# Performance work log

Measured on AMD Instinct MI355X. Metric: run time of the kernel, lower is better.

Reference implementation:

```python
import jax, jax.numpy as jnp
import numpy as np
import math

HEADS = 16
MAX_LEN = 512  # tokens; seq must equal this for the relative bias to be valid
D_HEAD = 64
BH = 256  # batch*heads


def setup_inputs() -> dict:
    key = jax.random.key(0)
    k1, k2, k3, k4 = jax.random.split(key, 4)
    S, B, D = MAX_LEN, BH, D_HEAD
    return {
        "query": jax.random.normal(k1, (S, B, D), dtype=jnp.float32),
        "key": jax.random.normal(k2, (S, B, D), dtype=jnp.float32),
        "value": jax.random.normal(k3, (S, B, D), dtype=jnp.float32),
        # per-head relative position embedding table [heads, 2*tokens-1, d_head]
        "k_rpos_emb": jax.random.normal(k4, (HEADS, 2 * MAX_LEN - 1, D), dtype=jnp.float32),
    }


def reference(query, key, value, k_rpos_emb):
    # 'seq b f -> b seq f'
    q = jnp.transpose(query, (1, 0, 2))   # [bh, s, d]
    k = jnp.transpose(key, (1, 0, 2))
    v = jnp.transpose(value, (1, 0, 2))
    bh, s, d = q.shape
    b = bh // HEADS

    # relative position bias from keys: split heads, contract with per-head table
    kh = k.reshape(b, HEADS, s, d)                                   # [b,h,s,d]
    rel_logits = jnp.einsum('bhid,hrd->bhir', kh, k_rpos_emb)        # [b,h,s,2L-1]
    rel_idx = (jnp.arange(s)[None, :] - jnp.arange(s)[:, None]
               + MAX_LEN - 1).astype(jnp.int32)                      # [s,s] in [0,2L-2]
    rel_bias = jnp.take_along_axis(
        rel_logits, rel_idx[None, None, :, :], axis=-1)              # [b,h,s,s]
    rel_bias = rel_bias.reshape(bh, s, s)

    scale = 1.0 / math.sqrt(d)
    scores = (jnp.einsum('bid,bjd->bij', q, k) + rel_bias) * scale   # [bh,s,s]
    attn = jax.nn.softmax(scores, axis=-1)
    out = jnp.einsum('bij,bjd->bid', attn, v)                        # [bh,s,d]
    return jnp.transpose(out, (1, 0, 2))                             # [s,bh,d]
```

## Files before the change

### kernel.cpp

```cpp
#include <hip/hip_runtime.h>
#include <hip/hip_bf16.h>

#define S_LEN  512
#define D_DIM  64
#define NH     16
#define R_LEN  1023
#define BHD    16384
#define PPITCH 68
#define SCL2   0.1803368801111204f
#define DTHR   8.0f

typedef __attribute__((ext_vector_type(8))) short   short8_t;
typedef __attribute__((ext_vector_type(8))) __bf16  bf16x8;
typedef __attribute__((ext_vector_type(4))) float   floatx4;

__device__ __forceinline__ unsigned short f2bf(float f) {
  union { float f; unsigned u; } v; v.f = f;
  return (unsigned short)((v.u + 0x7fffu + ((v.u >> 16) & 1u)) >> 16);
}
__device__ __forceinline__ ushort2 c2(float x, float y) {
  __hip_bfloat162 h = __float22bfloat162_rn(float2{x, y});
  union { __hip_bfloat162 h; ushort2 u; } v; v.h = h; return v.u;
}
__device__ __forceinline__ unsigned c2u(float x, float y) {
  ushort2 u = c2(x, y);
  union { ushort2 u; unsigned w; } v; v.u = u; return v.w;
}
__device__ __forceinline__ short8_t pack8s(float4 a, float4 b) {
  union { ushort2 u2[4]; short8_t s8; } u;
  u.u2[0] = c2(a.x, a.y); u.u2[1] = c2(a.z, a.w);
  u.u2[2] = c2(b.x, b.y); u.u2[3] = c2(b.z, b.w);
  return u.s8;
}
__device__ __forceinline__ bf16x8 pack8(float4 a, float4 b) {
  short8_t s = pack8s(a, b);
  return __builtin_bit_cast(bf16x8, s);
}
__device__ __forceinline__ bf16x8 pack8scaled(float4 a, float4 b, float s) {
  a.x *= s; a.y *= s; a.z *= s; a.w *= s;
  b.x *= s; b.y *= s; b.z *= s; b.w *= s;
  return pack8(a, b);
}
__device__ __forceinline__ bf16x8 ldfrag(const unsigned short* p) {
  short8_t s = *(const short8_t*)p;
  return __builtin_bit_cast(bf16x8, s);
}
__device__ __forceinline__ bf16x8 ldfrag8(const unsigned short* p) {
  union { ushort4 u4[2]; short8_t s8; } u;
  u.u4[0] = *(const ushort4*)p;
  u.u4[1] = *(const ushort4*)(p + 4);
  return __builtin_bit_cast(bf16x8, u.s8);
}
__device__ __forceinline__ bf16x8 ldseg(const unsigned short* buf, int r, int seg) {
  return ldfrag(buf + r * 64 + ((seg ^ (r & 7)) << 3));
}
__device__ __forceinline__ void async16(const void* g, void* l) {
  __builtin_amdgcn_global_load_lds(
      (const __attribute__((address_space(1))) unsigned int*)(unsigned long long)(uintptr_t)g,
      (__attribute__((address_space(3))) unsigned int*)(unsigned int)(uintptr_t)l,
      16, 0, 0);
}
__device__ __forceinline__ void stage16(const unsigned short* gb, size_t rstride,
                                        unsigned short* lb, int lane) {
  int srow = lane >> 3;
  int sseg = (lane & 7) ^ srow;
  async16(gb + (size_t)srow * rstride + sseg * 8, lb);
  async16(gb + (size_t)(srow + 8) * rstride + sseg * 8, lb + 512);
}
__device__ __forceinline__ void stageE(const unsigned short* gb, int sigma,
                                       unsigned short* slot, int lane, int wv) {
  int srow = lane >> 3;
  int sseg = (lane & 7) ^ srow;
  int r0 = sigma * 64 + wv * 16 + srow;
  unsigned short* lb = slot + (wv * 16) * 64;
  async16(gb + (size_t)min(r0, R_LEN - 1) * D_DIM + sseg * 8, lb);
  async16(gb + (size_t)min(r0 + 8, R_LEN - 1) * D_DIM + sseg * 8, lb + 512);
}
template<int N>
__device__ __forceinline__ float dpp_ror(float x) {
  int i = __builtin_bit_cast(int, x);
  int r = __builtin_amdgcn_update_dpp(i, i, 0x120 + N, 0xF, 0xF, false);
  return __builtin_bit_cast(float, r);
}
__device__ __forceinline__ float rmax16(float x) {
  x = fmaxf(x, dpp_ror<8>(x)); x = fmaxf(x, dpp_ror<4>(x));
  x = fmaxf(x, dpp_ror<2>(x)); x = fmaxf(x, dpp_ror<1>(x));
  return x;
}
__device__ __forceinline__ float rsum16(float x) {
  x += dpp_ror<8>(x); x += dpp_ror<4>(x);
  x += dpp_ror<2>(x); x += dpp_ror<1>(x);
  return x;
}
__device__ __forceinline__ float fexp2(float x) {
#if __has_builtin(__builtin_amdgcn_exp2f)
  return __builtin_amdgcn_exp2f(x);
#else
  return exp2f(x);
#endif
}

extern "C" __global__ void prepass(const float* __restrict__ k, const float* __restrict__ v,
                                   const float* __restrict__ emb,
                                   unsigned short* __restrict__ kb,
                                   unsigned short* __restrict__ vtb,
                                   unsigned short* __restrict__ eb) {
  __shared__ unsigned tw[64 * 36];
  const int bid = blockIdx.x;
  const int tid = threadIdx.x;
  if (bid < 4096) {
    size_t i = (size_t)bid * 256 + tid;
    const float* s = k + i * 8;
    float4 a = *(const float4*)s, b = *(const float4*)(s + 4);
    *(short8_t*)(kb + i * 8) = pack8s(a, b);
  } else if (bid < 4608) {
    size_t i = (size_t)(bid - 4096) * 256 + tid;
    if (i < 130944) {
      const float* s = emb + i * 8;
      float4 a = *(const float4*)s, b = *(const float4*)(s + 4);
      bf16x8 r = pack8scaled(a, b, SCL2);
      *(short8_t*)(eb + i * 8) = __builtin_bit_cast(short8_t, r);
    }
  } else {
    const int b2 = bid - 4608;
    const int bh = b2 >> 3;
    const int j0 = (b2 & 7) << 6;
    for (int item = tid; item < 512; item += 256) {
      const int dg = item & 15;
      const int jp = item >> 4;
      const float* s0 = v + (size_t)(j0 + 2 * jp) * BHD + bh * D_DIM + dg * 4;
      float4 a = *(const float4*)s0;
      float4 b = *(const float4*)(s0 + BHD);
      const unsigned key = (unsigned)(dg & 7);
      const unsigned col = (unsigned)(jp & 3) | ((((unsigned)jp >> 2) ^ key) << 2);
      tw[(dg * 4 + 0) * 36 + col] = c2u(a.x, b.x);
      tw[(dg * 4 + 1) * 36 + col] = c2u(a.y, b.y);
      tw[(dg * 4 + 2) * 36 + col] = c2u(a.z, b.z);
      tw[(dg * 4 + 3) * 36 + col] = c2u(a.w, b.w);
    }
    __syncthreads();
    for (int item = tid; item < 512; item += 256) {
      const int d = item >> 3, jseg = item & 7;
      const unsigned key = ((unsigned)d >> 2) & 7;
      const unsigned* p = tw + d * 36 + (((unsigned)jseg ^ key) << 2);
      uint4 w = *(const uint4*)p;
      *(uint4*)(vtb + ((size_t)bh * D_DIM + d) * S_LEN + j0 + jseg * 8) = w;
    }
  }
}

extern "C" __global__ __launch_bounds__(256, 2)
void attn_relbias(const float* __restrict__ q, const unsigned short* __restrict__ kb,
                  const unsigned short* __restrict__ vtb,
                  const unsigned short* __restrict__ eb,
                  float* __restrict__ out)
{
  __shared__ unsigned short kbuf[2][4096];
  __shared__ unsigned short vbuf[2][4096];
  __shared__ unsigned short ebuf[4][4096];
  __shared__ unsigned short ps[4][16 * PPITCH];

  const int tid  = threadIdx.x;
  const int bh   = blockIdx.x & 255;
  const int i0   = (blockIdx.x >> 8) << 7;
  const int h    = bh & (NH - 1);
  const int wv   = tid >> 6;
  const int lane = tid & 63;
  const int l15  = lane & 15;
  const int quad = lane >> 4;
  const int iloc0 = wv * 16 + quad * 4;
  const int elo   = 3 - wv;
  const int arow  = wv * 16 + l15;
  const int acol  = quad * 8;
  const int it0   = 7 - (i0 >> 6);

  const unsigned short* kgb  = kb  + (size_t)bh * D_DIM;
  const unsigned short* vgb  = vtb + (size_t)bh * (D_DIM * S_LEN);
  const unsigned short* egb  = eb  + (size_t)h * (R_LEN * D_DIM);

  stage16(kgb + (size_t)(wv * 16) * BHD, BHD, &kbuf[0][(wv * 16) * 64], lane);
  stage16(vgb + (size_t)(wv * 16) * S_LEN, S_LEN, &vbuf[0][(wv * 16) * 64], lane);
  stageE(egb, it0 - 1, ebuf[(it0 - 1) & 3], lane, wv);
  stageE(egb, it0,     ebuf[it0 & 3],       lane, wv);
  stageE(egb, it0 + 1, ebuf[(it0 + 1) & 3], lane, wv);

  bf16x8 qa0[2], qa1[2], ia0[2], ia1[2];
  #pragma unroll
  for (int st = 0; st < 2; ++st) {
    const int row = i0 + st * 64 + arow;
    const float* gq = q + (size_t)row * BHD + bh * D_DIM + acol;
    qa0[st] = pack8scaled(*(const float4*)gq,        *(const float4*)(gq + 4), SCL2);
    qa1[st] = pack8scaled(*(const float4*)(gq + 32), *(const float4*)(gq + 36), SCL2);
    const unsigned short* gi = kb + (size_t)row * BHD + bh * D_DIM + acol;
    ia0[st] = ldfrag(gi);
    ia1[st] = ldfrag(gi + 32);
  }

  floatx4 oacc[2][4];
  float m_i[2][4], l_i[2][4];
  #pragma unroll
  for (int st = 0; st < 2; ++st) {
    #pragma unroll
    for (int r = 0; r < 4; ++r) {
      oacc[st][r] = (floatx4){0.f, 0.f, 0.f, 0.f};
      m_i[st][r] = -1e30f; l_i[st][r] = 0.f;
    }
  }

  __syncthreads();

  #pragma unroll 2
  for (int t = 0; t < 8; ++t) {
    if (t < 7) {
      const int j1 = t * 64 + 64;
      stage16(kgb + (size_t)(j1 + wv * 16) * BHD, BHD, &kbuf[(t + 1) & 1][(wv * 16) * 64], lane);
      stage16(vgb + (size_t)(wv * 16) * S_LEN + j1, S_LEN, &vbuf[(t + 1) & 1][(wv * 16) * 64], lane);
      stageE(egb, it0 + t + 2, ebuf[(it0 + t + 2) & 3], lane, wv);
    }
    const unsigned short* kc = kbuf[t & 1];
    const unsigned short* vc = vbuf[t & 1];

    floatx4 bacc[2][5];
    floatx4 qk[2][4];
    __builtin_amdgcn_s_setprio(1);
    #pragma unroll
    for (int st = 0; st < 2; ++st) {
      const int sbase = it0 - st + t;
      #pragma unroll
      for (int ei = 0; ei < 5; ++ei) {
        const int eblk = elo + ei;
        const unsigned short* es = ebuf[(sbase + (eblk >> 2)) & 3];
        const int lr = (eblk * 16 + l15) & 63;
        floatx4 bz = (floatx4){0.f, 0.f, 0.f, 0.f};
        bz = __builtin_amdgcn_mfma_f32_16x16x32_bf16(ia0[st], ldseg(es, lr, quad),     bz, 0, 0, 0);
        bz = __builtin_amdgcn_mfma_f32_16x16x32_bf16(ia1[st], ldseg(es, lr, quad + 4), bz, 0, 0, 0);
        bacc[st][ei] = bz;
      }
    }
    #pragma unroll
    for (int c = 0; c < 4; ++c) {
      bf16x8 k0 = ldseg(kc, c * 16 + l15, quad);
      bf16x8 k1 = ldseg(kc, c * 16 + l15, quad + 4);
      #pragma unroll
      for (int st = 0; st < 2; ++st) {
        floatx4 acc = (floatx4){0.f, 0.f, 0.f, 0.f};
        acc = __builtin_amdgcn_mfma_f32_16x16x32_bf16(qa0[st], k0, acc, 0, 0, 0);
        acc = __builtin_amdgcn_mfma_f32_16x16x32_bf16(qa1[st], k1, acc, 0, 0, 0);
        qk[st][c] = acc;
      }
    }
    __builtin_amdgcn_s_setprio(0);

    unsigned short* psw = ps[wv];
    bf16x8 vb0[4], vb1[4];
    #pragma unroll
    for (int st = 0; st < 2; ++st) {
      float sc[4][4];
      #pragma unroll
      for (int r = 0; r < 4; ++r) {
        const int o  = 15 - 4 * quad - r;
        const int ls = (lane & 48) + ((l15 + o) & 15);
        const bool hi = (l15 + o) >= 16;
        #pragma unroll
        for (int c = 0; c < 4; ++c) {
          float blo = __shfl(bacc[st][c][r],     ls);
          float bhi = __shfl(bacc[st][c + 1][r], ls);
          sc[c][r] = qk[st][c][r] + (hi ? bhi : blo);
        }
      }
      float mx4[4];
      #pragma unroll
      for (int r = 0; r < 4; ++r) {
        float mx = fmaxf(fmaxf(sc[0][r], sc[1][r]), fmaxf(sc[2][r], sc[3][r]));
        mx4[r] = rmax16(mx);
      }
      float dm = fmaxf(fmaxf(mx4[0] - m_i[st][0], mx4[1] - m_i[st][1]),
                       fmaxf(mx4[2] - m_i[st][2], mx4[3] - m_i[st][3]));
      float p[4][4];
      if (__all(dm <= DTHR)) {
        #pragma unroll
        for (int r = 0; r < 4; ++r) {
          float rs = 0.f;
          #pragma unroll
          for (int c = 0; c < 4; ++c) { p[c][r] = fexp2(sc[c][r] - m_i[st][r]); rs += p[c][r]; }
          rs = rsum16(rs);
          l_i[st][r] += rs;
        }
      } else {
        #pragma unroll
        for (int r = 0; r < 4; ++r) {
          float mnew  = fmaxf(m_i[st][r], mx4[r]);
          float alpha = fexp2(m_i[st][r] - mnew);
          float rs = 0.f;
          #pragma unroll
          for (int c = 0; c < 4; ++c) { p[c][r] = fexp2(sc[c][r] - mnew); rs += p[c][r]; }
          rs = rsum16(rs);
          l_i[st][r] = l_i[st][r] * alpha + rs;
          m_i[st][r] = mnew;
          #pragma unroll
          for (int c = 0; c < 4; ++c) oacc[st][c][r] *= alpha;
        }
      }
      #pragma unroll
      for (int r = 0; r < 4; ++r) {
        ushort2 u01 = c2(p[0][r], p[1][r]);
        ushort2 u23 = c2(p[2][r], p[3][r]);
        unsigned short* pr = psw + (quad * 4 + r) * PPITCH + l15;
        pr[0]  = u01.x; pr[16] = u01.y; pr[32] = u23.x; pr[48] = u23.y;
      }
      bf16x8 pa0 = ldfrag8(psw + l15 * PPITCH + acol);
      bf16x8 pa1 = ldfrag8(psw + l15 * PPITCH + acol + 32);
      __builtin_amdgcn_s_setprio(1);
      #pragma unroll
      for (int c = 0; c < 4; ++c) {
        if (st == 0) {
          vb0[c] = ldseg(vc, c * 16 + l15, quad);
          vb1[c] = ldseg(vc, c * 16 + l15, quad + 4);
        }
        oacc[st][c] = __builtin_amdgcn_mfma_f32_16x16x32_bf16(pa0, vb0[c], oacc[st][c], 0, 0, 0);
        oacc[st][c] = __builtin_amdgcn_mfma_f32_16x16x32_bf16(pa1, vb1[c], oacc[st][c], 0, 0, 0);
      }
      __builtin_amdgcn_s_setprio(0);
    }

    __syncthreads();
  }

  #pragma unroll
  for (int st = 0; st < 2; ++st) {
    #pragma unroll
    for (int r = 0; r < 4; ++r) {
      float inv = 1.f / l_i[st][r];
      int row = i0 + st * 64 + iloc0 + r;
      #pragma unroll
      for (int c = 0; c < 4; ++c)
        out[(size_t)row * BHD + bh * D_DIM + c * 16 + l15] = oacc[st][c][r] * inv;
    }
  }
}

#define PITCH 72
extern "C" __global__ __launch_bounds__(256, 4)
void attn_fb(const float* __restrict__ q, const float* __restrict__ k,
             const float* __restrict__ v, const float* __restrict__ emb,
             float* __restrict__ out)
{
  __shared__ unsigned short kjs[64 * PITCH];
  __shared__ unsigned short vts[64 * PITCH];
  __shared__ unsigned short ps2[4][16 * PPITCH];

  const int tid  = threadIdx.x;
  const int bh   = blockIdx.x >> 3;
  const int i0   = (blockIdx.x & 7) << 6;
  const int h    = bh & (NH - 1);
  const int wv   = tid >> 6;
  const int lane = tid & 63;
  const int l15  = lane & 15;
  const int quad = lane >> 4;
  const int iloc0 = wv * 16 + quad * 4;
  const int elo   = 3 - wv;

  {
    const float* gq = q + (size_t)i0 * BHD + bh * D_DIM;
    const float* gk = k + (size_t)i0 * BHD + bh * D_DIM;
    for (int idx = tid; idx < 1024; idx += 256) {
      int row = idx >> 4, cg = (idx & 15) << 2;
      float4 a = *(const float4*)(gq + row * BHD + cg);
      float4 b = *(const float4*)(gk + row * BHD + cg);
      *(ushort4*)(vts + row * PITCH + cg) = (ushort4){ f2bf(a.x), f2bf(a.y), f2bf(a.z), f2bf(a.w) };
      *(ushort4*)(kjs + row * PITCH + cg) = (ushort4){ f2bf(b.x), f2bf(b.y), f2bf(b.z), f2bf(b.w) };
    }
  }
  __syncthreads();

  const int arow = wv * 16 + l15;
  const int acol = quad * 8;
  bf16x8 qa0 = ldfrag(vts + arow * PITCH + acol);
  bf16x8 qa1 = ldfrag(vts + arow * PITCH + acol + 32);
  bf16x8 ia0 = ldfrag(kjs + arow * PITCH + acol);
  bf16x8 ia1 = ldfrag(kjs + arow * PITCH + acol + 32);

  floatx4 oacc[4];
  #pragma unroll
  for (int c = 0; c < 4; ++c) oacc[c] = (floatx4){0.f, 0.f, 0.f, 0.f};
  float m_i[4] = { -1e30f, -1e30f, -1e30f, -1e30f };
  float l_i[4] = { 0.f, 0.f, 0.f, 0.f };

  for (int j0 = 0; j0 < S_LEN; j0 += 64) {
    __syncthreads();
    {
      const float* gk = k + (size_t)j0 * BHD + bh * D_DIM;
      for (int idx = tid; idx < 1024; idx += 256) {
        int row = idx >> 4, cg = (idx & 15) << 2;
        float4 b = *(const float4*)(gk + row * BHD + cg);
        *(ushort4*)(kjs + row * PITCH + cg) = (ushort4){ f2bf(b.x), f2bf(b.y), f2bf(b.z), f2bf(b.w) };
      }
    }
    {
      const float* gv = v + (size_t)j0 * BHD + bh * D_DIM;
      for (int idx = tid; idx < 1024; idx += 256) {
        int dg = idx & 15, jl = idx >> 4;
        float4 b = *(const float4*)(gv + jl * BHD + dg * 4);
        int d0 = dg * 4;
        vts[(d0 + 0) * PITCH + jl] = f2bf(b.x);
        vts[(d0 + 1) * PITCH + jl] = f2bf(b.y);
        vts[(d0 + 2) * PITCH + jl] = f2bf(b.z);
        vts[(d0 + 3) * PITCH + jl] = f2bf(b.w);
      }
    }
    floatx4 bacc[5];
    {
      const int rbase = j0 - i0 + 448;
      #pragma unroll
      for (int ei = 0; ei < 5; ++ei) {
        int rg = rbase + (elo + ei) * 16 + l15;
        rg = min(rg, R_LEN - 1);
        const float* ep = emb + ((size_t)h * R_LEN + rg) * D_DIM + acol;
        float4 e0 = *(const float4*)(ep);
        float4 e1 = *(const float4*)(ep + 4);
        float4 e2 = *(const float4*)(ep + 32);
        float4 e3 = *(const float4*)(ep + 36);
        floatx4 bz = (floatx4){0.f, 0.f, 0.f, 0.f};
        bz = __builtin_amdgcn_mfma_f32_16x16x32_bf16(ia0, pack8(e0, e1), bz, 0, 0, 0);
        bz = __builtin_amdgcn_mfma_f32_16x16x32_bf16(ia1, pack8(e2, e3), bz, 0, 0, 0);
        bacc[ei] = bz;
      }
    }
    __syncthreads();

    floatx4 qk[4];
    #pragma unroll
    for (int c = 0; c < 4; ++c) {
      bf16x8 kb0 = ldfrag(kjs + (c * 16 + l15) * PITCH + acol);
      bf16x8 kb1 = ldfrag(kjs + (c * 16 + l15) * PITCH + acol + 32);
      floatx4 acc = (floatx4){0.f, 0.f, 0.f, 0.f};
      acc = __builtin_amdgcn_mfma_f32_16x16x32_bf16(qa0, kb0, acc, 0, 0, 0);
      acc = __builtin_amdgcn_mfma_f32_16x16x32_bf16(qa1, kb1, acc, 0, 0, 0);
      qk[c] = acc;
    }
    float sc[4][4];
    #pragma unroll
    for (int r = 0; r < 4; ++r) {
      const int o  = 15 - 4 * quad - r;
      const int ls = (lane & 48) + ((l15 + o) & 15);
      const bool hi = (l15 + o) >= 16;
      #pragma unroll
      for (int c = 0; c < 4; ++c) {
        float blo = __shfl(bacc[c][r],     ls);
        float bhi = __shfl(bacc[c + 1][r], ls);
        sc[c][r] = (qk[c][r] + (hi ? bhi : blo)) * 0.125f;
      }
    }
    float p[4][4];
    #pragma unroll
    for (int r = 0; r < 4; ++r) {
      float mx = fmaxf(fmaxf(sc[0][r], sc[1][r]), fmaxf(sc[2][r], sc[3][r]));
      mx = rmax16(mx);
      float mnew  = fmaxf(m_i[r], mx);
      float alpha = __expf(m_i[r] - mnew);
      float rs = 0.f;
      #pragma unroll
      for (int c = 0; c < 4; ++c) { p[c][r] = __expf(sc[c][r] - mnew); rs += p[c][r]; }
      rs = rsum16(rs);
      l_i[r] = l_i[r] * alpha + rs;
      m_i[r] = mnew;
      #pragma unroll
      for (int c = 0; c < 4; ++c) oacc[c][r] *= alpha;
    }
    unsigned short* psw = ps2[wv];
    #pragma unroll
    for (int c = 0; c < 4; ++c) {
      #pragma unroll
      for (int r = 0; r < 4; ++r)
        psw[(quad * 4 + r) * PPITCH + c * 16 + l15] = f2bf(p[c][r]);
    }
    bf16x8 pa0 = ldfrag8(psw + l15 * PPITCH + acol);
    bf16x8 pa1 = ldfrag8(psw + l15 * PPITCH + acol + 32);
    #pragma unroll
    for (int c = 0; c < 4; ++c) {
      bf16x8 vb0 = ldfrag(vts + (c * 16 + l15) * PITCH + acol);
      bf16x8 vb1 = ldfrag(vts + (c * 16 + l15) * PITCH + acol + 32);
      oacc[c] = __builtin_amdgcn_mfma_f32_16x16x32_bf16(pa0, vb0, oacc[c], 0, 0, 0);
      oacc[c] = __builtin_amdgcn_mfma_f32_16x16x32_bf16(pa1, vb1, oacc[c], 0, 0, 0);
    }
  }
  #pragma unroll
  for (int r = 0; r < 4; ++r) {
    float inv = 1.f / l_i[r];
    int row = i0 + iloc0 + r;
    #pragma unroll
    for (int c = 0; c < 4; ++c)
      out[(size_t)row * BHD + bh * D_DIM + c * 16 + l15] = oacc[c][r] * inv;
  }
}

extern "C" void kernel_launch(void* const* d_in, const int* in_sizes, int n_in,
                              void* d_out, int out_size, void* d_ws, size_t ws_size,
                              hipStream_t stream) {
  const float* q   = (const float*)d_in[0];
  const float* k   = (const float*)d_in[1];
  const float* v   = (const float*)d_in[2];
  const float* emb = (const float*)d_in[3];
  float* out = (float*)d_out;

  const size_t kb_off  = 0;
  const size_t vtb_off = (size_t)512 * 256 * 64 * 2;
  const size_t eb_off  = vtb_off * 2;
  const size_t need    = eb_off + (size_t)NH * R_LEN * D_DIM * 2;

  if (ws_size >= need) {
    unsigned short* kbp  = (unsigned short*)((char*)d_ws + kb_off);
    unsigned short* vtbp = (unsigned short*)((char*)d_ws + vtb_off);
    unsigned short* ebp  = (unsigned short*)((char*)d_ws + eb_off);
    hipLaunchKernelGGL(prepass, dim3(6656), dim3(256), 0, stream, k, v, emb, kbp, vtbp, ebp);
    hipLaunchKernelGGL(attn_relbias, dim3(1024), dim3(256), 0, stream,
                       q, kbp, vtbp, ebp, out);
  } else {
    hipLaunchKernelGGL(attn_fb, dim3(2048), dim3(256), 0, stream, q, k, v, emb, out);
  }
}
```

Before: 202.0 us.

## Load K and V fragments directly from global memory, dropping LDS staging

```diff
diff --git a/kernel.cpp b/kernel.cpp
--- a/kernel.cpp
+++ b/kernel.cpp
@@ -59,13 +59,6 @@
       (const __attribute__((address_space(1))) unsigned int*)(unsigned long long)(uintptr_t)g,
       (__attribute__((address_space(3))) unsigned int*)(unsigned int)(uintptr_t)l,
       16, 0, 0);
-}
-__device__ __forceinline__ void stage16(const unsigned short* gb, size_t rstride,
-                                        unsigned short* lb, int lane) {
-  int srow = lane >> 3;
-  int sseg = (lane & 7) ^ srow;
-  async16(gb + (size_t)srow * rstride + sseg * 8, lb);
-  async16(gb + (size_t)(srow + 8) * rstride + sseg * 8, lb + 512);
 }
 __device__ __forceinline__ void stageE(const unsigned short* gb, int sigma,
                                        unsigned short* slot, int lane, int wv) {
@@ -112,7 +105,12 @@
     size_t i = (size_t)bid * 256 + tid;
     const float* s = k + i * 8;
     float4 a = *(const float4*)s, b = *(const float4*)(s + 4);
-    *(short8_t*)(kb + i * 8) = pack8s(a, b);
+    size_t e = i * 8;
+    int srow = (int)(e >> 14);
+    int rem  = (int)(e & 16383);
+    int bh   = rem >> 6;
+    int d    = rem & 63;
+    *(short8_t*)(kb + (size_t)bh * (S_LEN * D_DIM) + srow * D_DIM + d) = pack8s(a, b);
   } else if (bid < 4608) {
     size_t i = (size_t)(bid - 4096) * 256 + tid;
     if (i < 130944) {
@@ -149,14 +147,12 @@
   }
 }
 
-extern "C" __global__ __launch_bounds__(256, 2)
+extern "C" __global__ __launch_bounds__(256, 3)
 void attn_relbias(const float* __restrict__ q, const unsigned short* __restrict__ kb,
                   const unsigned short* __restrict__ vtb,
                   const unsigned short* __restrict__ eb,
                   float* __restrict__ out)
 {
-  __shared__ unsigned short kbuf[2][4096];
-  __shared__ unsigned short vbuf[2][4096];
   __shared__ unsigned short ebuf[4][4096];
   __shared__ unsigned short ps[4][16 * PPITCH];
 
@@ -174,12 +170,10 @@
   const int acol  = quad * 8;
   const int it0   = 7 - (i0 >> 6);
 
-  const unsigned short* kgb  = kb  + (size_t)bh * D_DIM;
+  const unsigned short* kgb  = kb  + (size_t)bh * (S_LEN * D_DIM);
   const unsigned short* vgb  = vtb + (size_t)bh * (D_DIM * S_LEN);
   const unsigned short* egb  = eb  + (size_t)h * (R_LEN * D_DIM);
 
-  stage16(kgb + (size_t)(wv * 16) * BHD, BHD, &kbuf[0][(wv * 16) * 64], lane);
-  stage16(vgb + (size_t)(wv * 16) * S_LEN, S_LEN, &vbuf[0][(wv * 16) * 64], lane);
   stageE(egb, it0 - 1, ebuf[(it0 - 1) & 3], lane, wv);
   stageE(egb, it0,     ebuf[it0 & 3],       lane, wv);
   stageE(egb, it0 + 1, ebuf[(it0 + 1) & 3], lane, wv);
@@ -191,7 +185,7 @@
     const float* gq = q + (size_t)row * BHD + bh * D_DIM + acol;
     qa0[st] = pack8scaled(*(const float4*)gq,        *(const float4*)(gq + 4), SCL2);
     qa1[st] = pack8scaled(*(const float4*)(gq + 32), *(const float4*)(gq + 36), SCL2);
-    const unsigned short* gi = kb + (size_t)row * BHD + bh * D_DIM + acol;
+    const unsigned short* gi = kgb + (size_t)row * D_DIM + acol;
     ia0[st] = ldfrag(gi);
     ia1[st] = ldfrag(gi + 32);
   }
@@ -211,14 +205,11 @@
 
   #pragma unroll 2
   for (int t = 0; t < 8; ++t) {
-    if (t < 7) {
-      const int j1 = t * 64 + 64;
-      stage16(kgb + (size_t)(j1 + wv * 16) * BHD, BHD, &kbuf[(t + 1) & 1][(wv * 16) * 64], lane);
-      stage16(vgb + (size_t)(wv * 16) * S_LEN + j1, S_LEN, &vbuf[(t + 1) & 1][(wv * 16) * 64], lane);
+    if (t < 7)
       stageE(egb, it0 + t + 2, ebuf[(it0 + t + 2) & 3], lane, wv);
-    }
-    const unsigned short* kc = kbuf[t & 1];
-    const unsigned short* vc = vbuf[t & 1];
+
+    const unsigned short* ktile = kgb + (size_t)t * (64 * D_DIM);
+    const unsigned short* vtile = vgb + t * 64;
 
     floatx4 bacc[2][5];
     floatx4 qk[2][4];
@@ -239,8 +230,9 @@
     }
     #pragma unroll
     for (int c = 0; c < 4; ++c) {
-      bf16x8 k0 = ldseg(kc, c * 16 + l15, quad);
-      bf16x8 k1 = ldseg(kc, c * 16 + l15, quad + 4);
+      const unsigned short* kr = ktile + (size_t)(c * 16 + l15) * D_DIM + acol;
+      bf16x8 k0 = ldfrag(kr);
+      bf16x8 k1 = ldfrag(kr + 32);
       #pragma unroll
       for (int st = 0; st < 2; ++st) {
         floatx4 acc = (floatx4){0.f, 0.f, 0.f, 0.f};
@@ -314,8 +306,9 @@
       #pragma unroll
       for (int c = 0; c < 4; ++c) {
         if (st == 0) {
-          vb0[c] = ldseg(vc, c * 16 + l15, quad);
-          vb1[c] = ldseg(vc, c * 16 + l15, quad + 4);
+          const unsigned short* vr = vtile + (size_t)(c * 16 + l15) * S_LEN + acol;
+          vb0[c] = ldfrag(vr);
+          vb1[c] = ldfrag(vr + 32);
         }
         oacc[st][c] = __builtin_amdgcn_mfma_f32_16x16x32_bf16(pa0, vb0[c], oacc[st][c], 0, 0, 0);
         oacc[st][c] = __builtin_amdgcn_mfma_f32_16x16x32_bf16(pa1, vb1[c], oacc[st][c], 0, 0, 0);
```

Result: slower. 332.7 us (+64.7%).
